# Kernel optimization log

Measured on AMD Instinct MI355X. Metric: run time of the kernel, lower is better.

The kernel has to match this reference:

```python
import jax, jax.numpy as jnp
import numpy as np

N_NODES = 100000
N_EDGES = 1600000
F_IN = 256
HID = 16
HEADS = 8
N_CLASSES = 16
NEG_SLOPE = 0.2  # DGL GATConv default leaky_relu slope


def setup_inputs() -> dict:
    key = jax.random.key(0)
    ks = jax.random.split(key, 12)
    feat = jax.random.normal(ks[0], (N_NODES, F_IN), dtype=jnp.float32)
    src = jax.random.randint(ks[1], (N_EDGES,), 0, N_NODES, dtype=jnp.int32)
    dst = jax.random.randint(ks[2], (N_EDGES,), 0, N_NODES, dtype=jnp.int32)
    s1 = 1.0 / np.sqrt(F_IN)
    s2 = 1.0 / np.sqrt(HID * HEADS)
    W1 = jax.random.normal(ks[3], (F_IN, HEADS * HID), dtype=jnp.float32) * s1
    al1 = jax.random.normal(ks[4], (HEADS, HID), dtype=jnp.float32) * s1
    ar1 = jax.random.normal(ks[5], (HEADS, HID), dtype=jnp.float32) * s1
    b1 = jnp.zeros((HEADS * HID,), dtype=jnp.float32)
    W2 = jax.random.normal(ks[6], (HEADS * HID, N_CLASSES), dtype=jnp.float32) * s2
    al2 = jax.random.normal(ks[7], (1, N_CLASSES), dtype=jnp.float32) * s2
    ar2 = jax.random.normal(ks[8], (1, N_CLASSES), dtype=jnp.float32) * s2
    b2 = jnp.zeros((N_CLASSES,), dtype=jnp.float32)
    return {"feat": feat, "src": src, "dst": dst,
            "W1": W1, "al1": al1, "ar1": ar1, "b1": b1,
            "W2": W2, "al2": al2, "ar2": ar2, "b2": b2}


def gat_conv(x, src, dst, W, attn_l, attn_r, bias, n_heads, out_dim):
    # x: [N, F_in]; W: [F_in, H*D]; attn_l/attn_r: [H, D]; bias: [H*D]
    n = x.shape[0]
    h = (x @ W).reshape(n, n_heads, out_dim)              # [N,H,D]
    el = jnp.einsum('nhd,hd->nh', h, attn_l)              # [N,H]
    er = jnp.einsum('nhd,hd->nh', h, attn_r)              # [N,H]
    e = jax.nn.leaky_relu(el[src] + er[dst], NEG_SLOPE)   # [E,H]
    # segment softmax over incoming edges of each destination node
    e_max = jax.ops.segment_max(e, dst, num_segments=n)   # [N,H] (-inf for isolated)
    ex = jnp.exp(e - e_max[dst])                          # [E,H]
    denom = jax.ops.segment_sum(ex, dst, num_segments=n)  # [N,H]
    a = ex / denom[dst]                                   # [E,H]
    msg = a[:, :, None] * h[src]                          # [E,H,D]
    out = jax.ops.segment_sum(msg, dst, num_segments=n)   # [N,H,D]
    return out + bias.reshape(1, n_heads, out_dim)


def reference(feat, src, dst, W1, al1, ar1, b1, W2, al2, ar2, b2):
    h = gat_conv(feat, src, dst, W1, al1, ar1, b1, HEADS, HID)   # [N,H,HID]
    h = jax.nn.elu(h.reshape(h.shape[0], -1))                     # [N,H*HID]
    h = gat_conv(h, src, dst, W2, al2, ar2, b2, 1, N_CLASSES)     # [N,1,C]
    h = h.reshape(h.shape[0], -1)
    return jax.nn.log_softmax(h, axis=1)
```

## Files before the change

### kernel.cpp

```cpp
#include <hip/hip_runtime.h>

#define N_NODES 100000
#define N_EDGES 1600000
#define F_IN 256
#define HD1 128
#define HEADS 8
#define HID 16
#define NC 16
#define NEG_SLOPE 0.2f
#define LOG2E 1.44269504f

#define BKT_NODES 512
#define NBKT ((N_NODES + BKT_NODES - 1) / BKT_NODES)
#define P1_EPB 8192
#define P1_BLOCKS ((N_EDGES + P1_EPB - 1) / P1_EPB)
#define SPLITW_BLOCKS ((F_IN * HD1) / 256)

__device__ __forceinline__ float leaky(float x){ return x > 0.f ? x : NEG_SLOPE * x; }
__device__ __forceinline__ unsigned short f2bf(float f){
    unsigned u = __float_as_uint(f);
    u += 0x7fff + ((u >> 16) & 1);
    return (unsigned short)(u >> 16);
}
__device__ __forceinline__ float bf2f(unsigned short s){
    return __uint_as_float((unsigned)s << 16);
}
__device__ __forceinline__ unsigned char f2fp8(float v){
    return (unsigned char)(__builtin_amdgcn_cvt_pk_fp8_f32(v, v, 0, false) & 0xff);
}
__device__ __forceinline__ unsigned cvtpk_bf16(float lo, float hi){
    unsigned r;
    asm("v_cvt_pk_bf16_f32 %0, %1, %2" : "=v"(r) : "v"(lo), "v"(hi));
    return r;
}

typedef __bf16 bf16x8 __attribute__((ext_vector_type(8)));
typedef short short8 __attribute__((ext_vector_type(8)));
typedef float f32x4 __attribute__((ext_vector_type(4)));
typedef float f32x2 __attribute__((ext_vector_type(2)));


__global__ void __launch_bounds__(256) k_p1hist(const int* __restrict__ dst, int* __restrict__ bucketPart,
                                                const float* __restrict__ W1, short* __restrict__ WTH){
    int t = threadIdx.x;
    int bid = blockIdx.x;
    if (bid >= P1_BLOCKS){
        int i = (bid - P1_BLOCKS) * 256 + t;
        int k = i >> 7, n = i & 127;
        int idx = n * 256 + (k ^ ((n & 7) << 3));
        WTH[idx] = (short)f2bf(W1[i]);
        return;
    }
    __shared__ int h[NBKT];
    for (int i = t; i < NBKT; i += 256) h[i] = 0;
    __syncthreads();
    int base = bid * P1_EPB;
    int m = min(P1_EPB, N_EDGES - base);
    for (int i = t; i < m; i += 256) atomicAdd(&h[(unsigned)dst[base + i] >> 9], 1);
    __syncthreads();
    for (int i = t; i < NBKT; i += 256) bucketPart[bid * NBKT + i] = h[i];
}

__global__ void __launch_bounds__(256) k_p1scan(const int* __restrict__ bucketPart,
                                                int* __restrict__ bucketBase, int* __restrict__ bucketCursor,
                                                int* __restrict__ off){
    __shared__ int sc[256];
    int t = threadIdx.x;
    int v = 0;
    if (t < NBKT)
        for (int b = 0; b < P1_BLOCKS; b++) v += bucketPart[b * NBKT + t];
    sc[t] = v; __syncthreads();
    for (int o = 1; o < 256; o <<= 1){
        int a = (t >= o) ? sc[t - o] : 0;
        __syncthreads();
        sc[t] += a;
        __syncthreads();
    }
    if (t < NBKT){
        int b = sc[t] - v;
        bucketBase[t] = b;
        bucketCursor[t] = b;
    }
    if (t == 0){ bucketBase[NBKT] = N_EDGES; off[N_NODES] = N_EDGES; }
}

__global__ void __launch_bounds__(256) k_p1bin(const int* __restrict__ src, const int* __restrict__ dst,
                                               const int* __restrict__ bucketPart,
                                               int* __restrict__ bucketCursor,
                                               unsigned long long* __restrict__ pairs){
    __shared__ unsigned long long pl[P1_EPB];
    __shared__ int h[NBKT];
    __shared__ int dl[NBKT];
    __shared__ int sc[256];
    int t = threadIdx.x;
    int bid = blockIdx.x;
    int v = (t < NBKT) ? bucketPart[bid * NBKT + t] : 0;
    sc[t] = v; __syncthreads();
    for (int o = 1; o < 256; o <<= 1){
        int a = (t >= o) ? sc[t - o] : 0;
        __syncthreads();
        sc[t] += a;
        __syncthreads();
    }
    if (t < NBKT){
        int ex = sc[t] - v;
        int gb = v ? atomicAdd(&bucketCursor[t], v) : 0;
        dl[t] = gb - ex;
        h[t] = ex;
    }
    __syncthreads();
    int base = bid * P1_EPB;
    int m = min(P1_EPB, N_EDGES - base);
    for (int i = t; i < m; i += 256){
        int d = dst[base + i], s = src[base + i];
        int b = (unsigned)d >> 9;
        int p = atomicAdd(&h[b], 1);
        pl[p] = ((unsigned long long)(unsigned)d << 32) | (unsigned)s;
    }
    __syncthreads();
    for (int i = t; i < m; i += 256){
        unsigned long long pr = pl[i];
        int b = (unsigned)(pr >> 32) >> 9;
        pairs[i + dl[b]] = pr;
    }
}

__global__ void __launch_bounds__(256) k_p2place(const unsigned long long* __restrict__ pairs,
                                                 const int* __restrict__ bucketBase,
                                                 int* __restrict__ off, int* __restrict__ csr_src){
    __shared__ int degc[BKT_NODES];
    __shared__ int sc2[BKT_NODES];
    int t = threadIdx.x;
    int b = blockIdx.x;
    int node0 = b * BKT_NODES;
    int nmax = min(BKT_NODES, N_NODES - node0);
    int p0 = bucketBase[b], p1 = bucketBase[b + 1];
    int m = p1 - p0;
    for (int i = t; i < BKT_NODES; i += 256) degc[i] = 0;
    __syncthreads();
    for (int i = t; i < m; i += 256){
        int d = (int)(pairs[p0 + i] >> 32) - node0;
        atomicAdd(&degc[d], 1);
    }
    __syncthreads();
    for (int i = t; i < BKT_NODES; i += 256) sc2[i] = degc[i];
    __syncthreads();
    for (int o = 1; o < BKT_NODES; o <<= 1){
        int i0 = t, i1 = t + 256;
        int a0 = (i0 >= o) ? sc2[i0 - o] : 0;
        int a1 = (i1 >= o) ? sc2[i1 - o] : 0;
        __syncthreads();
        sc2[i0] += a0; sc2[i1] += a1;
        __syncthreads();
    }
    for (int i = t; i < BKT_NODES; i += 256){
        int cur = p0 + sc2[i] - degc[i];
        if (i < nmax) off[node0 + i] = cur;
        degc[i] = cur;
    }
    __syncthreads();
    for (int i = t; i < m; i += 256){
        unsigned long long pr = pairs[p0 + i];
        int d = (int)(pr >> 32) - node0;
        int pos = atomicAdd(&degc[d], 1);
        csr_src[pos] = (int)(unsigned)pr;
    }
}


__device__ __forceinline__ short8 pack8(float4 f0, float4 f1){
    uint4 p;
    p.x = cvtpk_bf16(f0.x, f0.y);
    p.y = cvtpk_bf16(f0.z, f0.w);
    p.z = cvtpk_bf16(f1.x, f1.y);
    p.w = cvtpk_bf16(f1.z, f1.w);
    return __builtin_bit_cast(short8, p);
}

__global__ void __launch_bounds__(512, 4) k_gemm1m(const float* __restrict__ feat,
                                                   const short* __restrict__ WTH,
                                                   unsigned char* __restrict__ h1f8){
    __shared__ short sWH[F_IN * HD1];
    int t = threadIdx.x;
    {
        const short8* gh = (const short8*)WTH;
        short8* sh = (short8*)sWH;
        for (int i = t; i < 4096; i += 512) sh[i] = gh[i];
    }
    __syncthreads();

    int wid = t >> 6, lane = t & 63;
    int m16 = lane & 15, kg = lane >> 4;
    int rowb = blockIdx.x * 256 + wid * 32;

    f32x4 acc[2][8];
    #pragma unroll
    for (int a = 0; a < 2; a++)
        #pragma unroll
        for (int b = 0; b < 8; b++)
            acc[a][b] = (f32x4){0.f, 0.f, 0.f, 0.f};

    int r0 = rowb + m16;       if (r0 > N_NODES - 1) r0 = N_NODES - 1;
    int r1 = rowb + 16 + m16;  if (r1 > N_NODES - 1) r1 = N_NODES - 1;
    const float* fp0 = feat + (size_t)r0 * F_IN;
    const float* fp1 = feat + (size_t)r1 * F_IN;

    #pragma unroll
    for (int ks = 0; ks < 8; ks++){
        int kbase = ks * 32 + kg * 8;
        short8 a0, a1;
        {
            const float4* p = (const float4*)(fp0 + kbase);
            a0 = pack8(p[0], p[1]);
        }
        {
            const float4* p = (const float4*)(fp1 + kbase);
            a1 = pack8(p[0], p[1]);
        }
        bf16x8 AH0 = __builtin_bit_cast(bf16x8, a0);
        bf16x8 AH1 = __builtin_bit_cast(bf16x8, a1);
        __builtin_amdgcn_s_setprio(1);
        #pragma unroll
        for (int c = 0; c < 8; c++){
            int n = (c << 4) + m16;
            int kk = kbase ^ ((n & 7) << 3);
            bf16x8 bh = __builtin_bit_cast(bf16x8, *(const short8*)(sWH + n * 256 + kk));
            acc[0][c] = __builtin_amdgcn_mfma_f32_16x16x32_bf16(AH0, bh, acc[0][c], 0, 0, 0);
            acc[1][c] = __builtin_amdgcn_mfma_f32_16x16x32_bf16(AH1, bh, acc[1][c], 0, 0, 0);
        }
        __builtin_amdgcn_s_setprio(0);
    }

    #pragma unroll
    for (int rf = 0; rf < 2; rf++){
        #pragma unroll
        for (int c = 0; c < 8; c++){
            #pragma unroll
            for (int r = 0; r < 4; r++){
                int row = rowb + rf * 16 + kg * 4 + r;
                if (row < N_NODES){
                    int col = c * 16 + m16;
                    h1f8[(size_t)row * HD1 + col] = f2fp8(acc[rf][c][r]);
                }
            }
        }
    }
}


__global__ void __launch_bounds__(256) k_attn1(const unsigned char* __restrict__ h1f8,
                                               const float* __restrict__ al1, const float* __restrict__ ar1,
                                               unsigned short* __restrict__ el1b, float* __restrict__ er1){
    int i = blockIdx.x * 256 + threadIdx.x;
    if (i >= N_NODES * HEADS) return;
    int n = i >> 3, h = i & 7;
    uint4 hv = *(const uint4*)(h1f8 + (size_t)n * HD1 + h * HID);
    unsigned uu[4] = {hv.x, hv.y, hv.z, hv.w};
    float pe = 0.f, pr = 0.f;
    #pragma unroll
    for (int j = 0; j < 4; j++){
        unsigned u = uu[j];
        float x0 = __builtin_amdgcn_cvt_f32_fp8(u, 0);
        float x1 = __builtin_amdgcn_cvt_f32_fp8(u, 1);
        float x2 = __builtin_amdgcn_cvt_f32_fp8(u, 2);
        float x3 = __builtin_amdgcn_cvt_f32_fp8(u, 3);
        const float4 a = ((const float4*)(al1 + h * HID))[j];
        const float4 r = ((const float4*)(ar1 + h * HID))[j];
        pe += x0 * a.x + x1 * a.y + x2 * a.z + x3 * a.w;
        pr += x0 * r.x + x1 * r.y + x2 * r.z + x3 * r.w;
    }
    el1b[i] = f2bf(pe * LOG2E);
    er1[i] = pr * LOG2E;
}


__global__ void __launch_bounds__(256) k_agg1(const int* __restrict__ off, const int* __restrict__ csr_src,
                                              const unsigned short* __restrict__ el1b,
                                              const float* __restrict__ er1,
                                              const unsigned char* __restrict__ h1f8,
                                              const float* __restrict__ b1,
                                              unsigned short* __restrict__ x2b){
    int wid = threadIdx.x >> 6, lane = threadIdx.x & 63;
    int n = blockIdx.x * 4 + wid;
    if (n >= N_NODES) return;
    int jb = off[n], je = off[n + 1];
    int sub = lane >> 4;
    int q = lane & 15;
    int hh = q >> 1;
    float ern = er1[n * HEADS + hh];
    float a0=0.f,a1=0.f,a2=0.f,a3=0.f,a4=0.f,a5=0.f,a6=0.f,a7=0.f,wsum=0.f;

    #pragma unroll 4
    for (int j = jb; j < je; j += 4){
        int jj = j + sub;
        int jc = (jj < je) ? jj : je - 1;
        int s = csr_src[jc];
        float el = bf2f(el1b[s * HEADS + hh]);
        float wv = (jj < je) ? __builtin_amdgcn_exp2f(leaky(el + ern)) : 0.f;
        wsum += wv;
        uint2 u = *(const uint2*)(h1f8 + (((size_t)s) << 7) + (q << 3));
        f32x2 p0 = __builtin_amdgcn_cvt_pk_f32_fp8(u.x, 0);
        f32x2 p1 = __builtin_amdgcn_cvt_pk_f32_fp8(u.x, 1);
        f32x2 p2 = __builtin_amdgcn_cvt_pk_f32_fp8(u.y, 0);
        f32x2 p3 = __builtin_amdgcn_cvt_pk_f32_fp8(u.y, 1);
        a0 += wv * p0.x; a1 += wv * p0.y;
        a2 += wv * p1.x; a3 += wv * p1.y;
        a4 += wv * p2.x; a5 += wv * p2.y;
        a6 += wv * p3.x; a7 += wv * p3.y;
    }

    a0 += __shfl_xor(a0, 16); a0 += __shfl_xor(a0, 32);
    a1 += __shfl_xor(a1, 16); a1 += __shfl_xor(a1, 32);
    a2 += __shfl_xor(a2, 16); a2 += __shfl_xor(a2, 32);
    a3 += __shfl_xor(a3, 16); a3 += __shfl_xor(a3, 32);
    a4 += __shfl_xor(a4, 16); a4 += __shfl_xor(a4, 32);
    a5 += __shfl_xor(a5, 16); a5 += __shfl_xor(a5, 32);
    a6 += __shfl_xor(a6, 16); a6 += __shfl_xor(a6, 32);
    a7 += __shfl_xor(a7, 16); a7 += __shfl_xor(a7, 32);
    wsum += __shfl_xor(wsum, 16); wsum += __shfl_xor(wsum, 32);

    if (sub == 0){
        float inv = (je > jb) ? 1.f / wsum : 0.f;
        float o0 = a0*inv, o1 = a1*inv, o2 = a2*inv, o3 = a3*inv;
        float o4 = a4*inv, o5 = a5*inv, o6 = a6*inv, o7 = a7*inv;
        float4 bv0 = *(const float4*)(b1 + (q << 3));
        float4 bv1 = *(const float4*)(b1 + (q << 3) + 4);
        o0 += bv0.x; o1 += bv0.y; o2 += bv0.z; o3 += bv0.w;
        o4 += bv1.x; o5 += bv1.y; o6 += bv1.z; o7 += bv1.w;
        o0 = o0 > 0.f ? o0 : __expf(o0) - 1.f;
        o1 = o1 > 0.f ? o1 : __expf(o1) - 1.f;
        o2 = o2 > 0.f ? o2 : __expf(o2) - 1.f;
        o3 = o3 > 0.f ? o3 : __expf(o3) - 1.f;
        o4 = o4 > 0.f ? o4 : __expf(o4) - 1.f;
        o5 = o5 > 0.f ? o5 : __expf(o5) - 1.f;
        o6 = o6 > 0.f ? o6 : __expf(o6) - 1.f;
        o7 = o7 > 0.f ? o7 : __expf(o7) - 1.f;
        uint4 ov;
        ov.x = cvtpk_bf16(o0, o1);
        ov.y = cvtpk_bf16(o2, o3);
        ov.z = cvtpk_bf16(o4, o5);
        ov.w = cvtpk_bf16(o6, o7);
        *(uint4*)(x2b + (size_t)n * HD1 + (q << 3)) = ov;
    }
}


__global__ void __launch_bounds__(256) k_gemm2(const unsigned short* __restrict__ x2b, const float* __restrict__ W2,
                                               const float* __restrict__ al2, const float* __restrict__ ar2,
                                               unsigned short* __restrict__ h2e, float* __restrict__ er2){
    __shared__ float sW[HD1 * NC];
    __shared__ float sX[16 * HD1];
    int t = threadIdx.x;
    for (int i = t; i < (HD1 * NC) / 4; i += 256)
        ((float4*)sW)[i] = ((const float4*)W2)[i];
    int r = t >> 4, c = t & 15;
    float a2 = al2[c], r2 = ar2[c];
    for (int g = blockIdx.x; g * 16 < N_NODES; g += gridDim.x){
        int rowb = g * 16;
        __syncthreads();
        {
            ushort4 v = ((const ushort4*)(x2b + (size_t)rowb * HD1))[t * 2];
            ushort4 v2 = ((const ushort4*)(x2b + (size_t)rowb * HD1))[t * 2 + 1];
            float4 f0 = { bf2f(v.x), bf2f(v.y), bf2f(v.z), bf2f(v.w) };
            float4 f1 = { bf2f(v2.x), bf2f(v2.y), bf2f(v2.z), bf2f(v2.w) };
            ((float4*)sX)[t * 2] = f0;
            ((float4*)sX)[t * 2 + 1] = f1;
        }
        __syncthreads();
        float acc = 0.f;
        #pragma unroll 8
        for (int k = 0; k < HD1; k++)
            acc += sX[r * HD1 + k] * sW[k * NC + c];
        int row = rowb + r;
        h2e[(size_t)row * 32 + c] = f2bf(acc);
        float pe = acc * a2, pr = acc * r2;
        #pragma unroll
        for (int d = 1; d < 16; d <<= 1){ pe += __shfl_xor(pe, d); pr += __shfl_xor(pr, d); }
        if (c == 0){
            *(float*)(h2e + (size_t)row * 32 + 16) = pe * LOG2E;
            er2[row] = pr * LOG2E;
        }
    }
}


__global__ void __launch_bounds__(256) k_agg2(const int* __restrict__ off, const int* __restrict__ csr_src,
                                              const float* __restrict__ er2,
                                              const unsigned short* __restrict__ h2e, const float* __restrict__ b2,
                                              float* __restrict__ out){
    int t = threadIdx.x;
    int sub = t >> 4;
    int c = t & 15;
    int n = blockIdx.x * 16 + sub;
    if (n >= N_NODES) return;
    int jb = off[n], je = off[n + 1];
    float er = er2[n];
    float accA = 0.f, accB = 0.f, wsA = 0.f, wsB = 0.f;
    int j = jb;
    #pragma unroll 2
    for (; j + 1 < je; j += 2){
        int s0 = csr_src[j];
        int s1 = csr_src[j + 1];
        const unsigned short* r0 = h2e + (size_t)s0 * 32;
        const unsigned short* r1 = h2e + (size_t)s1 * 32;
        float el0 = *(const float*)(r0 + 16);
        float el1 = *(const float*)(r1 + 16);
        float w0 = __builtin_amdgcn_exp2f(leaky(el0 + er));
        float w1 = __builtin_amdgcn_exp2f(leaky(el1 + er));
        float v0 = bf2f(r0[c]);
        float v1 = bf2f(r1[c]);
        wsA += w0; accA += w0 * v0;
        wsB += w1; accB += w1 * v1;
    }
    if (j < je){
        int s0 = csr_src[j];
        const unsigned short* r0 = h2e + (size_t)s0 * 32;
        float el0 = *(const float*)(r0 + 16);
        float w0 = __builtin_amdgcn_exp2f(leaky(el0 + er));
        wsA += w0; accA += w0 * bf2f(r0[c]);
    }
    float acc = accA + accB, wsum = wsA + wsB;
    float o = (je > jb) ? acc / wsum : 0.f;
    o += b2[c];
    float m = o;
    #pragma unroll
    for (int d = 1; d < 16; d <<= 1) m = fmaxf(m, __shfl_xor(m, d));
    float ex = __expf(o - m);
    #pragma unroll
    for (int d = 1; d < 16; d <<= 1) ex += __shfl_xor(ex, d);
    out[(size_t)n * NC + c] = o - m - __logf(ex);
}


extern "C" void kernel_launch(void* const* d_in, const int* in_sizes, int n_in,
                              void* d_out, int out_size, void* d_ws, size_t ws_size,
                              hipStream_t stream){
    const float* feat = (const float*)d_in[0];
    const int*   src  = (const int*)d_in[1];
    const int*   dst  = (const int*)d_in[2];
    const float* W1   = (const float*)d_in[3];
    const float* al1  = (const float*)d_in[4];
    const float* ar1  = (const float*)d_in[5];
    const float* b1   = (const float*)d_in[6];
    const float* W2   = (const float*)d_in[7];
    const float* al2  = (const float*)d_in[8];
    const float* ar2  = (const float*)d_in[9];
    const float* b2   = (const float*)d_in[10];
    float* out = (float*)d_out;

    char* w = (char*)d_ws;
    auto alloc = [&](size_t bytes) -> char* {
        char* p = w;
        w += (bytes + 255) & ~(size_t)255;
        return p;
    };
    int*   off      = (int*)alloc((size_t)(N_NODES + 1) * 4);
    int*   csr_src  = (int*)alloc((size_t)N_EDGES * 4);
    unsigned long long* pairs = (unsigned long long*)alloc((size_t)N_EDGES * 8);
    int*   bucketPart   = (int*)alloc((size_t)P1_BLOCKS * NBKT * 4);
    int*   bucketBase   = (int*)alloc((size_t)(NBKT + 1) * 4);
    int*   bucketCursor = (int*)alloc((size_t)(NBKT + 1) * 4);
    unsigned char*  h1f8 = (unsigned char*)alloc((size_t)N_NODES * HD1);
    unsigned short* el1b = (unsigned short*)alloc((size_t)N_NODES * HEADS * 2);
    float* er1v    = (float*)alloc((size_t)N_NODES * HEADS * 4);
    unsigned short* x2b = (unsigned short*)alloc((size_t)N_NODES * HD1 * 2);
    unsigned short* h2e = (unsigned short*)alloc((size_t)N_NODES * 64);
    float* er2v    = (float*)alloc((size_t)N_NODES * 4);
    short* WTH     = (short*)alloc((size_t)F_IN * HD1 * 2);

    k_p1hist<<<P1_BLOCKS + SPLITW_BLOCKS, 256, 0, stream>>>(dst, bucketPart, W1, WTH);
    k_p1scan<<<1, 256, 0, stream>>>(bucketPart, bucketBase, bucketCursor, off);
    k_p1bin<<<P1_BLOCKS, 256, 0, stream>>>(src, dst, bucketPart, bucketCursor, pairs);
    k_p2place<<<NBKT, 256, 0, stream>>>(pairs, bucketBase, off, csr_src);

    k_gemm1m<<<(N_NODES + 255) / 256, 512, 0, stream>>>(feat, WTH, h1f8);
    k_attn1<<<(N_NODES * HEADS + 255) / 256, 256, 0, stream>>>(h1f8, al1, ar1, el1b, er1v);

    k_agg1<<<(N_NODES + 3) / 4, 256, 0, stream>>>(off, csr_src, el1b, er1v, h1f8, b1, x2b);

    k_gemm2<<<1024, 256, 0, stream>>>(x2b, W2, al2, ar2, h2e, er2v);
    k_agg2<<<(N_NODES + 15) / 16, 256, 0, stream>>>(off, csr_src, er2v, h2e, b2, out);
}
```

Baseline: 204.5 us.

## Merge independent graph-binning and GEMM/attention kernels into shared launches

Horizontally fuses the edge binning pass with the layer-1 GEMM into one launch, and the CSR placement pass with the attention-score kernel into another, dispatching on block index. This removes two kernel launches and lets independent graph-build and dense work run concurrently on different CUs. In exchange, the binning blocks now run at 512 threads and carry the GEMM's large shared-memory footprint (about 68 KB), which may cut their occupancy.

Result: faster. 190.1 us, median of 2 (-7.1%).

```diff
diff --git a/kernel.cpp b/kernel.cpp
--- a/kernel.cpp
+++ b/kernel.cpp
@@ -15,6 +15,8 @@
 #define P1_EPB 8192
 #define P1_BLOCKS ((N_EDGES + P1_EPB - 1) / P1_EPB)
 #define SPLITW_BLOCKS ((F_IN * HD1) / 256)
+#define GEMM1_BLOCKS ((N_NODES + 255) / 256)
+#define ATTN1_BLOCKS ((N_NODES * HEADS + 255) / 256)
 
 __device__ __forceinline__ float leaky(float x){ return x > 0.f ? x : NEG_SLOPE * x; }
 __device__ __forceinline__ unsigned short f2bf(float f){
@@ -84,89 +86,6 @@
     if (t == 0){ bucketBase[NBKT] = N_EDGES; off[N_NODES] = N_EDGES; }
 }
 
-__global__ void __launch_bounds__(256) k_p1bin(const int* __restrict__ src, const int* __restrict__ dst,
-                                               const int* __restrict__ bucketPart,
-                                               int* __restrict__ bucketCursor,
-                                               unsigned long long* __restrict__ pairs){
-    __shared__ unsigned long long pl[P1_EPB];
-    __shared__ int h[NBKT];
-    __shared__ int dl[NBKT];
-    __shared__ int sc[256];
-    int t = threadIdx.x;
-    int bid = blockIdx.x;
-    int v = (t < NBKT) ? bucketPart[bid * NBKT + t] : 0;
-    sc[t] = v; __syncthreads();
-    for (int o = 1; o < 256; o <<= 1){
-        int a = (t >= o) ? sc[t - o] : 0;
-        __syncthreads();
-        sc[t] += a;
-        __syncthreads();
-    }
-    if (t < NBKT){
-        int ex = sc[t] - v;
-        int gb = v ? atomicAdd(&bucketCursor[t], v) : 0;
-        dl[t] = gb - ex;
-        h[t] = ex;
-    }
-    __syncthreads();
-    int base = bid * P1_EPB;
-    int m = min(P1_EPB, N_EDGES - base);
-    for (int i = t; i < m; i += 256){
-        int d = dst[base + i], s = src[base + i];
-        int b = (unsigned)d >> 9;
-        int p = atomicAdd(&h[b], 1);
-        pl[p] = ((unsigned long long)(unsigned)d << 32) | (unsigned)s;
-    }
-    __syncthreads();
-    for (int i = t; i < m; i += 256){
-        unsigned long long pr = pl[i];
-        int b = (unsigned)(pr >> 32) >> 9;
-        pairs[i + dl[b]] = pr;
-    }
-}
-
-__global__ void __launch_bounds__(256) k_p2place(const unsigned long long* __restrict__ pairs,
-                                                 const int* __restrict__ bucketBase,
-                                                 int* __restrict__ off, int* __restrict__ csr_src){
-    __shared__ int degc[BKT_NODES];
-    __shared__ int sc2[BKT_NODES];
-    int t = threadIdx.x;
-    int b = blockIdx.x;
-    int node0 = b * BKT_NODES;
-    int nmax = min(BKT_NODES, N_NODES - node0);
-    int p0 = bucketBase[b], p1 = bucketBase[b + 1];
-    int m = p1 - p0;
-    for (int i = t; i < BKT_NODES; i += 256) degc[i] = 0;
-    __syncthreads();
-    for (int i = t; i < m; i += 256){
-        int d = (int)(pairs[p0 + i] >> 32) - node0;
-        atomicAdd(&degc[d], 1);
-    }
-    __syncthreads();
-    for (int i = t; i < BKT_NODES; i += 256) sc2[i] = degc[i];
-    __syncthreads();
-    for (int o = 1; o < BKT_NODES; o <<= 1){
-        int i0 = t, i1 = t + 256;
-        int a0 = (i0 >= o) ? sc2[i0 - o] : 0;
-        int a1 = (i1 >= o) ? sc2[i1 - o] : 0;
-        __syncthreads();
-        sc2[i0] += a0; sc2[i1] += a1;
-        __syncthreads();
-    }
-    for (int i = t; i < BKT_NODES; i += 256){
-        int cur = p0 + sc2[i] - degc[i];
-        if (i < nmax) off[node0 + i] = cur;
-        degc[i] = cur;
-    }
-    __syncthreads();
-    for (int i = t; i < m; i += 256){
-        unsigned long long pr = pairs[p0 + i];
-        int d = (int)(pr >> 32) - node0;
-        int pos = atomicAdd(&degc[d], 1);
-        csr_src[pos] = (int)(unsigned)pr;
-    }
-}
-
 
 __device__ __forceinline__ short8 pack8(float4 f0, float4 f1){
     uint4 p;
@@ -177,11 +96,56 @@
     return __builtin_bit_cast(short8, p);
 }
 
-__global__ void __launch_bounds__(512, 4) k_gemm1m(const float* __restrict__ feat,
-                                                   const short* __restrict__ WTH,
-                                                   unsigned char* __restrict__ h1f8){
-    __shared__ short sWH[F_IN * HD1];
-    int t = threadIdx.x;
+__global__ void __launch_bounds__(512, 4) k_bin_gemm(const int* __restrict__ src, const int* __restrict__ dst,
+                                                     const int* __restrict__ bucketPart,
+                                                     int* __restrict__ bucketCursor,
+                                                     unsigned long long* __restrict__ pairs,
+                                                     const float* __restrict__ feat,
+                                                     const short* __restrict__ WTH,
+                                                     unsigned char* __restrict__ h1f8){
+    __shared__ __align__(16) char smem[69888];
+    int t = threadIdx.x;
+    int bid = blockIdx.x;
+
+    if (bid < P1_BLOCKS){
+        unsigned long long* pl = (unsigned long long*)smem;
+        int* h  = (int*)(smem + 65536);
+        int* dl = h + 256;
+        int* sc = dl + 256;
+        int v = (t < NBKT) ? bucketPart[bid * NBKT + t] : 0;
+        if (t < 256) sc[t] = v;
+        __syncthreads();
+        for (int o = 1; o < 256; o <<= 1){
+            int a = (t < 256 && t >= o) ? sc[t - o] : 0;
+            __syncthreads();
+            if (t < 256) sc[t] += a;
+            __syncthreads();
+        }
+        if (t < NBKT){
+            int ex = sc[t] - v;
+            int gb = v ? atomicAdd(&bucketCursor[t], v) : 0;
+            dl[t] = gb - ex;
+            h[t] = ex;
+        }
+        __syncthreads();
+        int base = bid * P1_EPB;
+        int m = min(P1_EPB, N_EDGES - base);
+        for (int i = t; i < m; i += 512){
+            int d = dst[base + i], s = src[base + i];
+            int b = (unsigned)d >> 9;
+            int p = atomicAdd(&h[b], 1);
+            pl[p] = ((unsigned long long)(unsigned)d << 32) | (unsigned)s;
+        }
+        __syncthreads();
+        for (int i = t; i < m; i += 512){
+            unsigned long long pr = pl[i];
+            int b = (unsigned)(pr >> 32) >> 9;
+            pairs[i + dl[b]] = pr;
+        }
+        return;
+    }
+
+    short* sWH = (short*)smem;
     {
         const short8* gh = (const short8*)WTH;
         short8* sh = (short8*)sWH;
@@ -191,7 +155,7 @@
 
     int wid = t >> 6, lane = t & 63;
     int m16 = lane & 15, kg = lane >> 4;
-    int rowb = blockIdx.x * 256 + wid * 32;
+    int rowb = (bid - P1_BLOCKS) * 256 + wid * 32;
 
     f32x4 acc[2][8];
     #pragma unroll
@@ -248,29 +212,75 @@
 }
 
 
-__global__ void __launch_bounds__(256) k_attn1(const unsigned char* __restrict__ h1f8,
-                                               const float* __restrict__ al1, const float* __restrict__ ar1,
-                                               unsigned short* __restrict__ el1b, float* __restrict__ er1){
-    int i = blockIdx.x * 256 + threadIdx.x;
-    if (i >= N_NODES * HEADS) return;
-    int n = i >> 3, h = i & 7;
-    uint4 hv = *(const uint4*)(h1f8 + (size_t)n * HD1 + h * HID);
-    unsigned uu[4] = {hv.x, hv.y, hv.z, hv.w};
-    float pe = 0.f, pr = 0.f;
-    #pragma unroll
-    for (int j = 0; j < 4; j++){
-        unsigned u = uu[j];
-        float x0 = __builtin_amdgcn_cvt_f32_fp8(u, 0);
-        float x1 = __builtin_amdgcn_cvt_f32_fp8(u, 1);
-        float x2 = __builtin_amdgcn_cvt_f32_fp8(u, 2);
-        float x3 = __builtin_amdgcn_cvt_f32_fp8(u, 3);
-        const float4 a = ((const float4*)(al1 + h * HID))[j];
-        const float4 r = ((const float4*)(ar1 + h * HID))[j];
-        pe += x0 * a.x + x1 * a.y + x2 * a.z + x3 * a.w;
-        pr += x0 * r.x + x1 * r.y + x2 * r.z + x3 * r.w;
-    }
-    el1b[i] = f2bf(pe * LOG2E);
-    er1[i] = pr * LOG2E;
+__global__ void __launch_bounds__(256) k_place_attn(const unsigned long long* __restrict__ pairs,
+                                                    const int* __restrict__ bucketBase,
+                                                    int* __restrict__ off, int* __restrict__ csr_src,
+                                                    const unsigned char* __restrict__ h1f8,
+                                                    const float* __restrict__ al1, const float* __restrict__ ar1,
+                                                    unsigned short* __restrict__ el1b, float* __restrict__ er1){
+    int t = threadIdx.x;
+    int bid = blockIdx.x;
+
+    if (bid >= NBKT){
+        int i = (bid - NBKT) * 256 + t;
+        if (i >= N_NODES * HEADS) return;
+        int n = i >> 3, h = i & 7;
+        uint4 hv = *(const uint4*)(h1f8 + (size_t)n * HD1 + h * HID);
+        unsigned uu[4] = {hv.x, hv.y, hv.z, hv.w};
+        float pe = 0.f, pr = 0.f;
+        #pragma unroll
+        for (int j = 0; j < 4; j++){
+            unsigned u = uu[j];
+            float x0 = __builtin_amdgcn_cvt_f32_fp8(u, 0);
+            float x1 = __builtin_amdgcn_cvt_f32_fp8(u, 1);
+            float x2 = __builtin_amdgcn_cvt_f32_fp8(u, 2);
+            float x3 = __builtin_amdgcn_cvt_f32_fp8(u, 3);
+            const float4 a = ((const float4*)(al1 + h * HID))[j];
+            const float4 r = ((const float4*)(ar1 + h * HID))[j];
+            pe += x0 * a.x + x1 * a.y + x2 * a.z + x3 * a.w;
+            pr += x0 * r.x + x1 * r.y + x2 * r.z + x3 * r.w;
+        }
+        el1b[i] = f2bf(pe * LOG2E);
+        er1[i] = pr * LOG2E;
+        return;
+    }
+
+    __shared__ int degc[BKT_NODES];
+    __shared__ int sc2[BKT_NODES];
+    int b = bid;
+    int node0 = b * BKT_NODES;
+    int nmax = min(BKT_NODES, N_NODES - node0);
+    int p0 = bucketBase[b], p1 = bucketBase[b + 1];
+    int m = p1 - p0;
+    for (int i = t; i < BKT_NODES; i += 256) degc[i] = 0;
+    __syncthreads();
+    for (int i = t; i < m; i += 256){
+        int d = (int)(pairs[p0 + i] >> 32) - node0;
+        atomicAdd(&degc[d], 1);
+    }
+    __syncthreads();
+    for (int i = t; i < BKT_NODES; i += 256) sc2[i] = degc[i];
+    __syncthreads();
+    for (int o = 1; o < BKT_NODES; o <<= 1){
+        int i0 = t, i1 = t + 256;
+        int a0 = (i0 >= o) ? sc2[i0 - o] : 0;
+        int a1 = (i1 >= o) ? sc2[i1 - o] : 0;
+        __syncthreads();
+        sc2[i0] += a0; sc2[i1] += a1;
+        __syncthreads();
+    }
+    for (int i = t; i < BKT_NODES; i += 256){
+        int cur = p0 + sc2[i] - degc[i];
+        if (i < nmax) off[node0 + i] = cur;
+        degc[i] = cur;
+    }
+    __syncthreads();
+    for (int i = t; i < m; i += 256){
+        unsigned long long pr = pairs[p0 + i];
+        int d = (int)(pr >> 32) - node0;
+        int pos = atomicAdd(&degc[d], 1);
+        csr_src[pos] = (int)(unsigned)pr;
+    }
 }
 
 
@@ -470,14 +480,11 @@
 
     k_p1hist<<<P1_BLOCKS + SPLITW_BLOCKS, 256, 0, stream>>>(dst, bucketPart, W1, WTH);
     k_p1scan<<<1, 256, 0, stream>>>(bucketPart, bucketBase, bucketCursor, off);
-    k_p1bin<<<P1_BLOCKS, 256, 0, stream>>>(src, dst, bucketPart, bucketCursor, pairs);
-    k_p2place<<<NBKT, 256, 0, stream>>>(pairs, bucketBase, off, csr_src);
-
-    k_gemm1m<<<(N_NODES + 255) / 256, 512, 0, stream>>>(feat, WTH, h1f8);
-    k_attn1<<<(N_NODES * HEADS + 255) / 256, 256, 0, stream>>>(h1f8, al1, ar1, el1b, er1v);
-
+    k_bin_gemm<<<P1_BLOCKS + GEMM1_BLOCKS, 512, 0, stream>>>(src, dst, bucketPart, bucketCursor, pairs,
+                                                             feat, WTH, h1f8);
+    k_place_attn<<<NBKT + ATTN1_BLOCKS, 256, 0, stream>>>(pairs, bucketBase, off, csr_src,
+                                                          h1f8, al1, ar1, el1b, er1v);
     k_agg1<<<(N_NODES + 3) / 4, 256, 0, stream>>>(off, csr_src, el1b, er1v, h1f8, b1, x2b);
-
     k_gemm2<<<1024, 256, 0, stream>>>(x2b, W2, al2, ar2, h2e, er2v);
     k_agg2<<<(N_NODES + 15) / 16, 256, 0, stream>>>(off, csr_src, er2v, h2e, b2, out);
 }
```
